# Kernel tuning notes

Measured on AMD Instinct MI355X. Metric: run time of the kernel, lower is better.

Reference implementation:

```python
import math
import jax, jax.numpy as jnp
import numpy as np

H = 16
D_MODEL = 1024
D_K = D_MODEL // H


def setup_inputs() -> dict:
    key = jax.random.key(0)
    ks = jax.random.split(key, 12)
    B, S = 4, 2048
    scale = 1.0 / math.sqrt(D_MODEL)
    inp = {
        "query": jax.random.normal(ks[0], (B, S, D_MODEL), jnp.float32),
        "key": jax.random.normal(ks[1], (B, S, D_MODEL), jnp.float32),
        "value": jax.random.normal(ks[2], (B, S, D_MODEL), jnp.float32),
        "mask": jnp.ones((B, 1, 1, S), jnp.int32),
        "Wq": jax.random.normal(ks[3], (D_MODEL, D_MODEL), jnp.float32) * scale,
        "bq": jnp.zeros((D_MODEL,), jnp.float32),
        "Wk": jax.random.normal(ks[4], (D_MODEL, D_MODEL), jnp.float32) * scale,
        "bk": jnp.zeros((D_MODEL,), jnp.float32),
        "Wv": jax.random.normal(ks[5], (D_MODEL, D_MODEL), jnp.float32) * scale,
        "bv": jnp.zeros((D_MODEL,), jnp.float32),
        "Wo": jax.random.normal(ks[6], (D_MODEL, D_MODEL), jnp.float32) * scale,
        "bo": jnp.zeros((D_MODEL,), jnp.float32),
    }
    return inp


def _split_heads(x, W, b):
    # x: (B, S, d_model) -> (B, H, S, d_k); torch Linear: x @ W.T + b
    B, S, _ = x.shape
    y = x @ W.T + b
    return y.reshape(B, S, H, D_K).transpose(0, 2, 1, 3)


def reference(query, key, value, mask, Wq, bq, Wk, bk, Wv, bv, Wo, bo):
    B, Sq, _ = query.shape
    q = _split_heads(query, Wq, bq)   # (B,H,Sq,dk)
    k = _split_heads(key, Wk, bk)     # (B,H,Skv,dk)
    v = _split_heads(value, Wv, bv)   # (B,H,Skv,dk)
    scores = jnp.einsum('bhqd,bhkd->bhqk', q, k) / math.sqrt(D_K)
    scores = jnp.where(mask == 0, jnp.float32(-1e9), scores)
    p_attn = jax.nn.softmax(scores, axis=-1)  # dropout p=0 (eval)
    x = jnp.einsum('bhqk,bhkd->bhqd', p_attn, v)
    x = x.transpose(0, 2, 1, 3).reshape(B, Sq, H * D_K)
    return x @ Wo.T + bo
```

## Files before the change

### kernel.cpp

```cpp
#include <hip/hip_runtime.h>
#include <hip/hip_bf16.h>
#include <stdint.h>

typedef unsigned short u16;
typedef short bf16x8 __attribute__((ext_vector_type(8)));
typedef float f32x4 __attribute__((ext_vector_type(4)));

#define D_MODEL 1024
#define NHEAD 16
#define DK 64
#define SEQ 2048
#define NB 4
#define MTOT (NB * SEQ)

__device__ __forceinline__ u16 f2bf(float f) {
  union { float f; unsigned u; } x; x.f = f;
  unsigned r = x.u + 0x7FFFu + ((x.u >> 16) & 1u);
  return (u16)(r >> 16);
}
#if __has_builtin(__builtin_amdgcn_cvt_pk_bf16_f32)
__device__ __forceinline__ unsigned pkbf(float a, float b) {
  auto r = __builtin_amdgcn_cvt_pk_bf16_f32(a, b);
  union { decltype(r) v; unsigned u; } c; c.v = r; return c.u;
}
#else
__device__ __forceinline__ unsigned pkbf(float a, float b) {
  return (unsigned)f2bf(a) | ((unsigned)f2bf(b) << 16);
}
#endif
#if __has_builtin(__builtin_amdgcn_exp2f)
__device__ __forceinline__ float exp2r(float x) { return __builtin_amdgcn_exp2f(x); }
#else
__device__ __forceinline__ float exp2r(float x) { return exp2f(x); }
#endif
__device__ __forceinline__ void gl_lds16(const u16* g, u16* s) {
  __builtin_amdgcn_global_load_lds(
      (const __attribute__((address_space(1))) void*)g,
      (__attribute__((address_space(3))) void*)s, 16, 0, 0);
}

struct CvtArgs {
  const float4* s[7];
  uint2* d[7];
  int n4[7];
};
__global__ __launch_bounds__(256) void cvt_all(CvtArgs a) {
  const int y = blockIdx.y;
  const float4* s = a.s[y];
  uint2* d = a.d[y];
  const int n4 = a.n4[y];
  for (int i = blockIdx.x * 256 + threadIdx.x; i < n4; i += gridDim.x * 256) {
    float4 x = s[i];
    uint2 o;
    o.x = pkbf(x.x, x.y);
    o.y = pkbf(x.z, x.w);
    d[i] = o;
  }
}

template <int MODE>
__device__ __forceinline__ void gemm_body(
    const u16* __restrict__ A, const u16* __restrict__ W,
    const float* __restrict__ bias, void* __restrict__ out, float scale,
    int m0, int n0, u16* smem)
{
  u16* As = smem;
  u16* Bs = smem + 8192;

  const int tid = threadIdx.x;
  const int l = tid & 63, w = tid >> 6;
  const int wm = (w >> 1) << 6, wn = (w & 1) << 6;

  int srow[4], sk8[4], sdst[4];
#pragma unroll
  for (int r = 0; r < 4; ++r) {
    int c = r * 256 + tid;
    srow[r] = c >> 3;
    sk8[r] = (c & 7) ^ (srow[r] & 7);
    sdst[r] = c << 3;
  }
  int aoff[4][2], boff[4][2];
#pragma unroll
  for (int i = 0; i < 4; ++i) {
    int mr = wm + (i << 4) + (l & 15);
    int nr = wn + (i << 4) + (l & 15);
#pragma unroll
    for (int s = 0; s < 2; ++s) {
      int kc = (s << 2) + (l >> 4);
      aoff[i][s] = (mr << 6) + ((kc ^ (mr & 7)) << 3);
      boff[i][s] = (nr << 6) + ((kc ^ (nr & 7)) << 3);
    }
  }

  const u16* Ab = A + (size_t)m0 * D_MODEL;
  const u16* Bb = W + (size_t)n0 * D_MODEL;

  f32x4 acc[4][4] = {};

  for (int kt = 0; kt < 16; ++kt) {
    const int kbase = kt << 6;
#pragma unroll
    for (int r = 0; r < 4; ++r)
      gl_lds16(Ab + (size_t)srow[r] * D_MODEL + kbase + (sk8[r] << 3), As + sdst[r]);
#pragma unroll
    for (int r = 0; r < 4; ++r)
      gl_lds16(Bb + (size_t)srow[r] * D_MODEL + kbase + (sk8[r] << 3), Bs + sdst[r]);
    __syncthreads();
#pragma unroll
    for (int s = 0; s < 2; ++s) {
      bf16x8 af[4], bfv[4];
#pragma unroll
      for (int i = 0; i < 4; ++i) af[i] = *(const bf16x8*)(As + aoff[i][s]);
#pragma unroll
      for (int j = 0; j < 4; ++j) bfv[j] = *(const bf16x8*)(Bs + boff[j][s]);
#pragma unroll
      for (int i = 0; i < 4; ++i)
#pragma unroll
        for (int j = 0; j < 4; ++j)
          acc[i][j] = __builtin_amdgcn_mfma_f32_16x16x32_bf16(af[i], bfv[j], acc[i][j], 0, 0, 0);
    }
    __syncthreads();
  }

  if (MODE == 1) {
    u16* Cs = smem;
    u16* outb = (u16*)out;
#pragma unroll
    for (int i = 0; i < 4; ++i)
#pragma unroll
      for (int j = 0; j < 4; ++j) {
        int sl = wm + (i << 4) + ((l >> 4) << 2);
        int nl = wn + (j << 4) + (l & 15);
        float bj = bias[n0 + nl];
        uint2 pk;
        pk.x = pkbf(acc[i][j][0] + bj, acc[i][j][1] + bj);
        pk.y = pkbf(acc[i][j][2] + bj, acc[i][j][3] + bj);
        *(uint2*)(Cs + nl * 136 + sl) = pk;
      }
    __syncthreads();
    int nl = tid >> 1, sh = (tid & 1) << 6;
    int n = n0 + nl;
    int b_ = m0 >> 11;
    const uint4* src = (const uint4*)(Cs + nl * 136 + sh);
    uint4* dst = (uint4*)(outb +
        (((size_t)b_ * NHEAD + (n >> 6)) * DK + (n & 63)) * SEQ + (m0 & 2047) + sh);
#pragma unroll
    for (int e = 0; e < 8; ++e) dst[e] = src[e];
  } else {
    u16* outb = (u16*)out;
    float* outf = (float*)out;
#pragma unroll
    for (int i = 0; i < 4; ++i)
#pragma unroll
      for (int j = 0; j < 4; ++j) {
        int ml = m0 + wm + (i << 4) + ((l >> 4) << 2);
        int n = n0 + wn + (j << 4) + (l & 15);
        float bj = bias[n];
#pragma unroll
        for (int r = 0; r < 4; ++r) {
          int m = ml + r;
          float v = (acc[i][j][r] + bj) * scale;
          if (MODE == 0)
            outb[(((size_t)(m >> 11) * NHEAD + (n >> 6)) * SEQ + (m & 2047)) * DK + (n & 63)] = f2bf(v);
          else
            outf[(size_t)m * D_MODEL + n] = v;
        }
      }
  }
}

template <int MODE>
__global__ __launch_bounds__(256) void gemm128(
    const u16* __restrict__ A, const u16* __restrict__ W,
    const float* __restrict__ bias, void* __restrict__ out, float scale)
{
  __shared__ alignas(16) u16 smem[17408];
  gemm_body<MODE>(A, W, bias, out, scale,
                  blockIdx.x << 7, blockIdx.y << 7, smem);
}

__global__ __launch_bounds__(256) void proj_qkv(
    const u16* __restrict__ Cq, const u16* __restrict__ Ck, const u16* __restrict__ Cv,
    const u16* __restrict__ wq, const u16* __restrict__ wk, const u16* __restrict__ wv,
    const float* __restrict__ bq, const float* __restrict__ bk, const float* __restrict__ bv,
    u16* __restrict__ Qb, u16* __restrict__ Kb, u16* __restrict__ Vt, float scq)
{
  __shared__ alignas(16) u16 smem[17408];
  const int z = blockIdx.z;
  const int m0 = blockIdx.x << 7, n0 = blockIdx.y << 7;
  if (z == 0)
    gemm_body<0>(Cq, wq, bq, Qb, scq, m0, n0, smem);
  else if (z == 1)
    gemm_body<0>(Ck, wk, bk, Kb, 1.0f, m0, n0, smem);
  else
    gemm_body<1>(Cv, wv, bv, Vt, 1.0f, m0, n0, smem);
}

__global__ __launch_bounds__(512, 4) void attn_fused(
    const u16* __restrict__ Q,
    const u16* __restrict__ K,
    const u16* __restrict__ Vt,
    const int* __restrict__ mask,
    u16* __restrict__ X)
{
  __shared__ alignas(16) u16 PQ[16384];
  __shared__ alignas(16) u16 Ks[2][4096];
  __shared__ alignas(16) u16 Vs[2][4096];
  __shared__ alignas(16) float mbf[2][64];

  const int tid = threadIdx.x;
  const int l = tid & 63, w = tid >> 6;
  const int lq = l & 15, qd = l >> 4;
  const int bh = blockIdx.x;
  const int q0 = blockIdx.y << 8;
  const int b_ = bh >> 4, h = bh & 15;
  const size_t base = (size_t)bh * SEQ * DK;
  const int wq0 = w << 5;

#pragma unroll
  for (int r = 0; r < 4; ++r) {
    int c = r * 512 + tid;
    int row = c >> 3, k8 = (c & 7) ^ (row & 7);
    gl_lds16(Q + base + (size_t)(q0 + row) * DK + (k8 << 3), PQ + (c << 3));
  }
  const int srow = tid >> 3, sk8 = (tid & 7) ^ (srow & 7);
  const u16* Kst = K + base + (size_t)srow * DK + (sk8 << 3);
  const u16* Vst = Vt + base + (size_t)srow * SEQ + (sk8 << 3);
  gl_lds16(Kst, Ks[0] + (tid << 3));
  gl_lds16(Vst, Vs[0] + (tid << 3));
  if (tid < 64) mbf[0][tid] = mask[b_ * SEQ + tid] ? 0.0f : -1.44269504e9f;
  __syncthreads();

  bf16x8 qf[2][2];
#pragma unroll
  for (int i = 0; i < 2; ++i)
#pragma unroll
    for (int s = 0; s < 2; ++s) {
      int row = wq0 + (i << 4) + lq;
      qf[i][s] = *(const bf16x8*)(PQ + (row << 6) + ((((s << 2) + qd) ^ (row & 7)) << 3));
    }

  const short onev = (lq == 0) ? (short)0x3F80 : (short)0;
  const bf16x8 onef = {onev, onev, onev, onev, onev, onev, onev, onev};

  f32x4 Ov[2][4] = {};
  f32x4 Ovl[2] = {};

  for (int t = 0; t < 32; ++t) {
    const int cur = t & 1;
    if (t + 1 < 32) {
      const int kv1 = (t + 1) << 6;
      gl_lds16(Kst + (size_t)kv1 * DK, Ks[cur ^ 1] + (tid << 3));
      gl_lds16(Vst + kv1, Vs[cur ^ 1] + (tid << 3));
      if (tid < 64) mbf[cur ^ 1][tid] = mask[b_ * SEQ + kv1 + tid] ? 0.0f : -1.44269504e9f;
    }

    const u16* Kc = Ks[cur];
    const u16* Vc = Vs[cur];

    f32x4 Sc[2][4];
#pragma unroll
    for (int jb = 0; jb < 4; ++jb) {
      float4 m4 = *(const float4*)(mbf[cur] + (jb << 4) + (qd << 2));
      Sc[0][jb][0] = m4.x; Sc[0][jb][1] = m4.y;
      Sc[0][jb][2] = m4.z; Sc[0][jb][3] = m4.w;
      Sc[1][jb] = Sc[0][jb];
    }

#pragma unroll
    for (int s = 0; s < 2; ++s) {
      bf16x8 kf[4];
#pragma unroll
      for (int jb = 0; jb < 4; ++jb) {
        int row = (jb << 4) + lq;
        kf[jb] = *(const bf16x8*)(Kc + (row << 6) + ((((s << 2) + qd) ^ (row & 7)) << 3));
      }
#pragma unroll
      for (int i = 0; i < 2; ++i)
#pragma unroll
        for (int jb = 0; jb < 4; ++jb)
          Sc[i][jb] = __builtin_amdgcn_mfma_f32_16x16x32_bf16(kf[jb], qf[i][s], Sc[i][jb], 0, 0, 0);
    }

    union { uint4 u; bf16x8 v; } pfu[2][2];
#pragma unroll
    for (int i = 0; i < 2; ++i) {
      unsigned pkv[4][2];
#pragma unroll
      for (int jb = 0; jb < 4; ++jb) {
        pkv[jb][0] = pkbf(exp2r(Sc[i][jb][0]), exp2r(Sc[i][jb][1]));
        pkv[jb][1] = pkbf(exp2r(Sc[i][jb][2]), exp2r(Sc[i][jb][3]));
      }
#pragma unroll
      for (int s = 0; s < 2; ++s) {
        pfu[i][s].u.x = pkv[2 * s][0];     pfu[i][s].u.y = pkv[2 * s][1];
        pfu[i][s].u.z = pkv[2 * s + 1][0]; pfu[i][s].u.w = pkv[2 * s + 1][1];
      }
    }

#pragma unroll
    for (int s = 0; s < 2; ++s) {
      bf16x8 vfv[4];
#pragma unroll
      for (int j = 0; j < 4; ++j) {
        int row = (j << 4) + lq;
        int rsw = row & 7;
        uint2 c0 = *(const uint2*)(Vc + (row << 6) +
                    ((((s << 2) + (qd >> 1)) ^ rsw) << 3) + ((qd & 1) << 2));
        uint2 c1 = *(const uint2*)(Vc + (row << 6) +
                    ((((s << 2) + 2 + (qd >> 1)) ^ rsw) << 3) + ((qd & 1) << 2));
        union { uint4 u; bf16x8 v; } cv;
        cv.u.x = c0.x; cv.u.y = c0.y; cv.u.z = c1.x; cv.u.w = c1.y;
        vfv[j] = cv.v;
      }
#pragma unroll
      for (int i = 0; i < 2; ++i) {
#pragma unroll
        for (int j = 0; j < 4; ++j)
          Ov[i][j] = __builtin_amdgcn_mfma_f32_16x16x32_bf16(pfu[i][s].v, vfv[j], Ov[i][j], 0, 0, 0);
        Ovl[i] = __builtin_amdgcn_mfma_f32_16x16x32_bf16(pfu[i][s].v, onef, Ovl[i], 0, 0, 0);
      }
    }
    __syncthreads();
  }

#pragma unroll
  for (int i = 0; i < 2; ++i) {
    float inv[4];
#pragma unroll
    for (int r = 0; r < 4; ++r) inv[r] = 1.0f / Ovl[i][r];
#pragma unroll
    for (int r = 0; r < 4; ++r) {
      float sc_ = __shfl(inv[r], l & 48);
      int qrow = q0 + wq0 + (i << 4) + (qd << 2) + r;
#pragma unroll
      for (int j = 0; j < 4; ++j)
        X[((size_t)b_ * SEQ + qrow) * D_MODEL + (h << 6) + (j << 4) + lq] =
            f2bf(Ov[i][j][r] * sc_);
    }
  }
}

extern "C" void kernel_launch(void* const* d_in, const int* in_sizes, int n_in,
                              void* d_out, int out_size, void* d_ws, size_t ws_size,
                              hipStream_t stream) {
  const float* query = (const float*)d_in[0];
  const float* key_  = (const float*)d_in[1];
  const float* value = (const float*)d_in[2];
  const int* mask    = (const int*)d_in[3];
  const float* Wq = (const float*)d_in[4];
  const float* bq = (const float*)d_in[5];
  const float* Wk = (const float*)d_in[6];
  const float* bk = (const float*)d_in[7];
  const float* Wv = (const float*)d_in[8];
  const float* bv = (const float*)d_in[9];
  const float* Wo = (const float*)d_in[10];
  const float* bo = (const float*)d_in[11];

  u16* ws16 = (u16*)d_ws;
  const size_t WSZ = (size_t)D_MODEL * D_MODEL;
  const size_t ASZ = (size_t)MTOT * D_MODEL;
  const float SCQ = 0.125f * 1.44269504088896f;

  dim3 blk(256);
  dim3 gg(MTOT / 128, D_MODEL / 128);

  if (ws_size >= (size_t)(4 * WSZ + 4 * ASZ) * 2) {
    u16* wqc = ws16;
    u16* wkc = ws16 + WSZ;
    u16* wvc = ws16 + 2 * WSZ;
    u16* woc = ws16 + 3 * WSZ;
    u16* Cq  = ws16 + 4 * WSZ;
    u16* Ck  = ws16 + 4 * WSZ + ASZ;
    u16* Qb  = ws16 + 4 * WSZ + 2 * ASZ;
    u16* Kb  = ws16 + 4 * WSZ + 3 * ASZ;
    u16* Xb  = Cq;
    u16* Vtb = (u16*)d_out;
    u16* Cv  = (u16*)d_out + ASZ;

    CvtArgs ca;
    ca.s[0] = (const float4*)query; ca.d[0] = (uint2*)Cq;  ca.n4[0] = (int)(ASZ / 4);
    ca.s[1] = (const float4*)key_;  ca.d[1] = (uint2*)Ck;  ca.n4[1] = (int)(ASZ / 4);
    ca.s[2] = (const float4*)value; ca.d[2] = (uint2*)Cv;  ca.n4[2] = (int)(ASZ / 4);
    ca.s[3] = (const float4*)Wq;    ca.d[3] = (uint2*)wqc; ca.n4[3] = (int)(WSZ / 4);
    ca.s[4] = (const float4*)Wk;    ca.d[4] = (uint2*)wkc; ca.n4[4] = (int)(WSZ / 4);
    ca.s[5] = (const float4*)Wv;    ca.d[5] = (uint2*)wvc; ca.n4[5] = (int)(WSZ / 4);
    ca.s[6] = (const float4*)Wo;    ca.d[6] = (uint2*)woc; ca.n4[6] = (int)(WSZ / 4);

    cvt_all<<<dim3(512, 7), blk, 0, stream>>>(ca);
    proj_qkv<<<dim3(MTOT / 128, D_MODEL / 128, 3), blk, 0, stream>>>(
        Cq, Ck, Cv, wqc, wkc, wvc, bq, bk, bv, Qb, Kb, Vtb, SCQ);
    attn_fused<<<dim3(NB * NHEAD, SEQ / 256), dim3(512), 0, stream>>>(Qb, Kb, Vtb, mask, Xb);
    gemm128<2><<<gg, blk, 0, stream>>>(Xb, woc, bo, d_out, 1.0f);
  } else {
    u16* wqc = ws16;
    u16* wkc = ws16 + WSZ;
    u16* wvc = ws16 + 2 * WSZ;
    u16* woc = ws16 + 3 * WSZ;
    u16* C1  = ws16 + 4 * WSZ;
    u16* Qb  = ws16 + 4 * WSZ + ASZ;
    u16* Kb  = ws16 + 4 * WSZ + 2 * ASZ;
    u16* Xb  = C1;
    u16* Vtb = (u16*)d_out;

    CvtArgs cw;
    for (int i = 0; i < 7; ++i) { cw.s[i] = (const float4*)Wq; cw.d[i] = (uint2*)wqc; cw.n4[i] = 0; }
    cw.s[0] = (const float4*)Wq; cw.d[0] = (uint2*)wqc; cw.n4[0] = (int)(WSZ / 4);
    cw.s[1] = (const float4*)Wk; cw.d[1] = (uint2*)wkc; cw.n4[1] = (int)(WSZ / 4);
    cw.s[2] = (const float4*)Wv; cw.d[2] = (uint2*)wvc; cw.n4[2] = (int)(WSZ / 4);
    cw.s[3] = (const float4*)Wo; cw.d[3] = (uint2*)woc; cw.n4[3] = (int)(WSZ / 4);

    cvt_all<<<dim3(512, 4), blk, 0, stream>>>(cw);
    CvtArgs c1;
    c1.s[0] = (const float4*)query; c1.d[0] = (uint2*)C1; c1.n4[0] = (int)(ASZ / 4);
    cvt_all<<<dim3(1024, 1), blk, 0, stream>>>(c1);
    gemm128<0><<<gg, blk, 0, stream>>>(C1, wqc, bq, Qb, SCQ);
    c1.s[0] = (const float4*)key_;
    cvt_all<<<dim3(1024, 1), blk, 0, stream>>>(c1);
    gemm128<0><<<gg, blk, 0, stream>>>(C1, wkc, bk, Kb, 1.0f);
    c1.s[0] = (const float4*)value;
    cvt_all<<<dim3(1024, 1), blk, 0, stream>>>(c1);
    gemm128<1><<<gg, blk, 0, stream>>>(C1, wvc, bv, Vtb, 1.0f);
    attn_fused<<<dim3(NB * NHEAD, SEQ / 256), dim3(512), 0, stream>>>(Qb, Kb, Vtb, mask, Xb);
    gemm128<2><<<gg, blk, 0, stream>>>(Xb, woc, bo, d_out, 1.0f);
  }
}
```

Measured before the change: 349.0 us.

## Double KV tile per barrier, load Q directly to registers, add MFMA priority hints

The attention kernel now stages 128 keys/values per loop iteration (two 64-row halves) and halves the number of iterations and barriers. The Q tile is read straight from global memory into registers, which drops the 32KB LDS staging buffer, so LDS use stays about the same while the KV buffers double. s_setprio raises wave priority around the MFMA blocks to help interleave waves. The risks are uncoalesced Q reads and more registers in flight.

```diff
diff --git a/kernel.cpp b/kernel.cpp
--- a/kernel.cpp
+++ b/kernel.cpp
@@ -203,10 +203,9 @@
     const int* __restrict__ mask,
     u16* __restrict__ X)
 {
-  __shared__ alignas(16) u16 PQ[16384];
-  __shared__ alignas(16) u16 Ks[2][4096];
-  __shared__ alignas(16) u16 Vs[2][4096];
-  __shared__ alignas(16) float mbf[2][64];
+  __shared__ alignas(16) u16 Ks[2][2][4096];
+  __shared__ alignas(16) u16 Vs[2][2][4096];
+  __shared__ alignas(16) float mbf[2][128];
 
   const int tid = threadIdx.x;
   const int l = tid & 63, w = tid >> 6;
@@ -217,27 +216,24 @@
   const size_t base = (size_t)bh * SEQ * DK;
   const int wq0 = w << 5;
 
-#pragma unroll
-  for (int r = 0; r < 4; ++r) {
-    int c = r * 512 + tid;
-    int row = c >> 3, k8 = (c & 7) ^ (row & 7);
-    gl_lds16(Q + base + (size_t)(q0 + row) * DK + (k8 << 3), PQ + (c << 3));
-  }
   const int srow = tid >> 3, sk8 = (tid & 7) ^ (srow & 7);
   const u16* Kst = K + base + (size_t)srow * DK + (sk8 << 3);
   const u16* Vst = Vt + base + (size_t)srow * SEQ + (sk8 << 3);
-  gl_lds16(Kst, Ks[0] + (tid << 3));
-  gl_lds16(Vst, Vs[0] + (tid << 3));
-  if (tid < 64) mbf[0][tid] = mask[b_ * SEQ + tid] ? 0.0f : -1.44269504e9f;
-  __syncthreads();
+
+#pragma unroll
+  for (int hh = 0; hh < 2; ++hh) {
+    gl_lds16(Kst + (size_t)(hh * 64) * DK, Ks[0][hh] + (tid << 3));
+    gl_lds16(Vst + hh * 64, Vs[0][hh] + (tid << 3));
+  }
+  if (tid < 128) mbf[0][tid] = mask[b_ * SEQ + tid] ? 0.0f : -1.44269504e9f;
 
   bf16x8 qf[2][2];
 #pragma unroll
   for (int i = 0; i < 2; ++i)
 #pragma unroll
     for (int s = 0; s < 2; ++s) {
-      int row = wq0 + (i << 4) + lq;
-      qf[i][s] = *(const bf16x8*)(PQ + (row << 6) + ((((s << 2) + qd) ^ (row & 7)) << 3));
+      int row = q0 + wq0 + (i << 4) + lq;
+      qf[i][s] = *(const bf16x8*)(Q + base + (size_t)row * DK + (((s << 2) + qd) << 3));
     }
 
   const short onev = (lq == 0) ? (short)0x3F80 : (short)0;
@@ -246,79 +242,92 @@
   f32x4 Ov[2][4] = {};
   f32x4 Ovl[2] = {};
 
-  for (int t = 0; t < 32; ++t) {
+  __syncthreads();
+
+  for (int t = 0; t < 16; ++t) {
     const int cur = t & 1;
-    if (t + 1 < 32) {
-      const int kv1 = (t + 1) << 6;
-      gl_lds16(Kst + (size_t)kv1 * DK, Ks[cur ^ 1] + (tid << 3));
-      gl_lds16(Vst + kv1, Vs[cur ^ 1] + (tid << 3));
-      if (tid < 64) mbf[cur ^ 1][tid] = mask[b_ * SEQ + kv1 + tid] ? 0.0f : -1.44269504e9f;
-    }
-
-    const u16* Kc = Ks[cur];
-    const u16* Vc = Vs[cur];
-
-    f32x4 Sc[2][4];
-#pragma unroll
-    for (int jb = 0; jb < 4; ++jb) {
-      float4 m4 = *(const float4*)(mbf[cur] + (jb << 4) + (qd << 2));
-      Sc[0][jb][0] = m4.x; Sc[0][jb][1] = m4.y;
-      Sc[0][jb][2] = m4.z; Sc[0][jb][3] = m4.w;
-      Sc[1][jb] = Sc[0][jb];
-    }
-
-#pragma unroll
-    for (int s = 0; s < 2; ++s) {
-      bf16x8 kf[4];
+    if (t + 1 < 16) {
+      const int kv1 = (t + 1) << 7;
+#pragma unroll
+      for (int hh = 0; hh < 2; ++hh) {
+        gl_lds16(Kst + (size_t)(kv1 + hh * 64) * DK, Ks[cur ^ 1][hh] + (tid << 3));
+        gl_lds16(Vst + kv1 + hh * 64, Vs[cur ^ 1][hh] + (tid << 3));
+      }
+      if (tid < 128) mbf[cur ^ 1][tid] = mask[b_ * SEQ + kv1 + tid] ? 0.0f : -1.44269504e9f;
+    }
+
+#pragma unroll
+    for (int hh = 0; hh < 2; ++hh) {
+      const u16* Kc = Ks[cur][hh];
+      const u16* Vc = Vs[cur][hh];
+      const float* mrow = mbf[cur] + (hh << 6);
+
+      f32x4 Sc[2][4];
 #pragma unroll
       for (int jb = 0; jb < 4; ++jb) {
-        int row = (jb << 4) + lq;
-        kf[jb] = *(const bf16x8*)(Kc + (row << 6) + ((((s << 2) + qd) ^ (row & 7)) << 3));
-      }
-#pragma unroll
-      for (int i = 0; i < 2; ++i)
-#pragma unroll
-        for (int jb = 0; jb < 4; ++jb)
-          Sc[i][jb] = __builtin_amdgcn_mfma_f32_16x16x32_bf16(kf[jb], qf[i][s], Sc[i][jb], 0, 0, 0);
-    }
-
-    union { uint4 u; bf16x8 v; } pfu[2][2];
-#pragma unroll
-    for (int i = 0; i < 2; ++i) {
-      unsigned pkv[4][2];
-#pragma unroll
-      for (int jb = 0; jb < 4; ++jb) {
-        pkv[jb][0] = pkbf(exp2r(Sc[i][jb][0]), exp2r(Sc[i][jb][1]));
-        pkv[jb][1] = pkbf(exp2r(Sc[i][jb][2]), exp2r(Sc[i][jb][3]));
-      }
+        float4 m4 = *(const float4*)(mrow + (jb << 4) + (qd << 2));
+        Sc[0][jb][0] = m4.x; Sc[0][jb][1] = m4.y;
+        Sc[0][jb][2] = m4.z; Sc[0][jb][3] = m4.w;
+        Sc[1][jb] = Sc[0][jb];
+      }
+
 #pragma unroll
       for (int s = 0; s < 2; ++s) {
-        pfu[i][s].u.x = pkv[2 * s][0];     pfu[i][s].u.y = pkv[2 * s][1];
-        pfu[i][s].u.z = pkv[2 * s + 1][0]; pfu[i][s].u.w = pkv[2 * s + 1][1];
-      }
-    }
-
-#pragma unroll
-    for (int s = 0; s < 2; ++s) {
-      bf16x8 vfv[4];
-#pragma unroll
-      for (int j = 0; j < 4; ++j) {
-        int row = (j << 4) + lq;
-        int rsw = row & 7;
-        uint2 c0 = *(const uint2*)(Vc + (row << 6) +
-                    ((((s << 2) + (qd >> 1)) ^ rsw) << 3) + ((qd & 1) << 2));
-        uint2 c1 = *(const uint2*)(Vc + (row << 6) +
-                    ((((s << 2) + 2 + (qd >> 1)) ^ rsw) << 3) + ((qd & 1) << 2));
-        union { uint4 u; bf16x8 v; } cv;
-        cv.u.x = c0.x; cv.u.y = c0.y; cv.u.z = c1.x; cv.u.w = c1.y;
-        vfv[j] = cv.v;
-      }
+        bf16x8 kf[4];
+#pragma unroll
+        for (int jb = 0; jb < 4; ++jb) {
+          int row = (jb << 4) + lq;
+          kf[jb] = *(const bf16x8*)(Kc + (row << 6) + ((((s << 2) + qd) ^ (row & 7)) << 3));
+        }
+        __builtin_amdgcn_s_setprio(1);
+#pragma unroll
+        for (int i = 0; i < 2; ++i)
+#pragma unroll
+          for (int jb = 0; jb < 4; ++jb)
+            Sc[i][jb] = __builtin_amdgcn_mfma_f32_16x16x32_bf16(kf[jb], qf[i][s], Sc[i][jb], 0, 0, 0);
+        __builtin_amdgcn_s_setprio(0);
+      }
+
+      union { uint4 u; bf16x8 v; } pfu[2][2];
 #pragma unroll
       for (int i = 0; i < 2; ++i) {
-#pragma unroll
-        for (int j = 0; j < 4; ++j)
-          Ov[i][j] = __builtin_amdgcn_mfma_f32_16x16x32_bf16(pfu[i][s].v, vfv[j], Ov[i][j], 0, 0, 0);
-        Ovl[i] = __builtin_amdgcn_mfma_f32_16x16x32_bf16(pfu[i][s].v, onef, Ovl[i], 0, 0, 0);
+        unsigned pkv[4][2];
+#pragma unroll
+        for (int jb = 0; jb < 4; ++jb) {
+          pkv[jb][0] = pkbf(exp2r(Sc[i][jb][0]), exp2r(Sc[i][jb][1]));
+          pkv[jb][1] = pkbf(exp2r(Sc[i][jb][2]), exp2r(Sc[i][jb][3]));
+        }
+#pragma unroll
+        for (int s = 0; s < 2; ++s) {
+          pfu[i][s].u.x = pkv[2 * s][0];     pfu[i][s].u.y = pkv[2 * s][1];
+          pfu[i][s].u.z = pkv[2 * s + 1][0]; pfu[i][s].u.w = pkv[2 * s + 1][1];
+        }
+      }
+
+#pragma unroll
+      for (int s = 0; s < 2; ++s) {
+        bf16x8 vfv[4];
+#pragma unroll
+        for (int j = 0; j < 4; ++j) {
+          int row = (j << 4) + lq;
+          int rsw = row & 7;
+          uint2 c0 = *(const uint2*)(Vc + (row << 6) +
+                      ((((s << 2) + (qd >> 1)) ^ rsw) << 3) + ((qd & 1) << 2));
+          uint2 c1 = *(const uint2*)(Vc + (row << 6) +
+                      ((((s << 2) + 2 + (qd >> 1)) ^ rsw) << 3) + ((qd & 1) << 2));
+          union { uint4 u; bf16x8 v; } cv;
+          cv.u.x = c0.x; cv.u.y = c0.y; cv.u.z = c1.x; cv.u.w = c1.y;
+          vfv[j] = cv.v;
+        }
+        __builtin_amdgcn_s_setprio(1);
+#pragma unroll
+        for (int i = 0; i < 2; ++i) {
+#pragma unroll
+          for (int j = 0; j < 4; ++j)
+            Ov[i][j] = __builtin_amdgcn_mfma_f32_16x16x32_bf16(pfu[i][s].v, vfv[j], Ov[i][j], 0, 0, 0);
+          Ovl[i] = __builtin_amdgcn_mfma_f32_16x16x32_bf16(pfu[i][s].v, onef, Ovl[i], 0, 0, 0);
+        }
+        __builtin_amdgcn_s_setprio(0);
       }
     }
     __syncthreads();
```

Measured after the change: 344.6 us. About the same (-1.3%).
